# Kernel optimization log

Measured on AMD Instinct MI355X. Metric: run time of the kernel, lower is better.

Reference implementation:

```python
import jax, jax.numpy as jnp
import numpy as np

B, C, H, W = 32, 3, 512, 512


def setup_inputs() -> dict:
    key = jax.random.key(0)
    k_img, k_mask = jax.random.split(key)
    image = jax.random.normal(k_img, (B, C, H, W), dtype=jnp.float32)
    # mask values: 0 -> pepper (set 0.0), 1 -> salt (set 1.0), 2 -> keep pixel
    mask = jax.random.randint(k_mask, (B, 1, H, W), 0, 3, dtype=jnp.int32)
    return {"image": image, "mask": mask}


def reference(image, mask):
    # mask (B,1,H,W) broadcasts over channels, matching repeat(1, C, 1, 1).
    # Single fused elementwise pass: 0 where mask==0, 1 where mask==1, else image.
    out = jnp.where(mask == 0, jnp.float32(0.0),
                    jnp.where(mask == 1, jnp.float32(1.0), image))
    return out
```

## Files before the change

kernel.cpp:

```cpp
#include <hip/hip_runtime.h>


constexpr int B  = 32;
constexpr int C  = 3;
constexpr int HW = 512 * 512;
constexpr int G_PER_PLANE = HW / 4;
constexpr int TOTAL_G = B * C * G_PER_PLANE;
constexpr int U = 4;
constexpr int BLOCK = 256;
constexpr int G_PER_BLOCK = BLOCK * U;

typedef float nt_f4 __attribute__((ext_vector_type(4)));
typedef int   nt_i4 __attribute__((ext_vector_type(4)));

__global__ __launch_bounds__(BLOCK)
void sp_kernel(const float* __restrict__ img,
               const int*   __restrict__ mask,
               float*       __restrict__ out) {
    const int base = blockIdx.x * G_PER_BLOCK + threadIdx.x;

    int   t[U];
    nt_i4 m[U];
    nt_f4 v[U];

    #pragma unroll
    for (int k = 0; k < U; ++k) {
        t[k] = base + k * BLOCK;
        const int plane = t[k] >> 16;
        const int b     = plane / 3;
        const int g     = t[k] & (G_PER_PLANE - 1);
        m[k] = *(const nt_i4*)(mask + (size_t)b * HW + (size_t)g * 4);
        v[k] = *(const nt_f4*)(img + (size_t)t[k] * 4);
    }

    #pragma unroll
    for (int k = 0; k < U; ++k) {
        nt_f4 r;
        r.x = (m[k].x == 0) ? 0.0f : ((m[k].x == 1) ? 1.0f : v[k].x);
        r.y = (m[k].y == 0) ? 0.0f : ((m[k].y == 1) ? 1.0f : v[k].y);
        r.z = (m[k].z == 0) ? 0.0f : ((m[k].z == 1) ? 1.0f : v[k].z);
        r.w = (m[k].w == 0) ? 0.0f : ((m[k].w == 1) ? 1.0f : v[k].w);
        __builtin_nontemporal_store(r, (nt_f4*)(out + (size_t)t[k] * 4));
    }
}

extern "C" void kernel_launch(void* const* d_in, const int* in_sizes, int n_in,
                              void* d_out, int out_size, void* d_ws, size_t ws_size,
                              hipStream_t stream) {
    const float* img  = (const float*)d_in[0];
    const int*   mask = (const int*)d_in[1];
    float*       out  = (float*)d_out;

    const int grid = TOTAL_G / G_PER_BLOCK;
    sp_kernel<<<grid, BLOCK, 0, stream>>>(img, mask, out);
}
```

Baseline: 201.6 us.

## Use fixed 2048-block grid with per-thread loop and plain stores

Replaces the one-tile-per-block launch (6144 blocks) with a fixed grid of 2048 blocks, each looping over three unrolled tiles of four float4 groups per thread. This cuts block scheduling overhead and gives each thread more independent loads in flight. It also swaps the nontemporal output stores for ordinary stores. That may change cache behaviour for the 100MB write stream and could add L2 pollution.

```diff
diff --git a/kernel.cpp b/kernel.cpp
--- a/kernel.cpp
+++ b/kernel.cpp
@@ -6,41 +6,46 @@
 constexpr int HW = 512 * 512;
 constexpr int G_PER_PLANE = HW / 4;
 constexpr int TOTAL_G = B * C * G_PER_PLANE;
-constexpr int U = 4;
-constexpr int BLOCK = 256;
-constexpr int G_PER_BLOCK = BLOCK * U;
+constexpr int BLOCK   = 256;
+constexpr int GRID    = 2048;
+constexpr int G_PER_BLOCK = TOTAL_G / GRID;
+constexpr int U       = 4;
+constexpr int ITERS   = G_PER_BLOCK / (BLOCK * U);
 
-typedef float nt_f4 __attribute__((ext_vector_type(4)));
-typedef int   nt_i4 __attribute__((ext_vector_type(4)));
+typedef float f4 __attribute__((ext_vector_type(4)));
+typedef int   i4 __attribute__((ext_vector_type(4)));
 
 __global__ __launch_bounds__(BLOCK)
 void sp_kernel(const float* __restrict__ img,
                const int*   __restrict__ mask,
                float*       __restrict__ out) {
-    const int base = blockIdx.x * G_PER_BLOCK + threadIdx.x;
-
-    int   t[U];
-    nt_i4 m[U];
-    nt_f4 v[U];
+    const int blockBase = blockIdx.x * G_PER_BLOCK + threadIdx.x;
 
     #pragma unroll
-    for (int k = 0; k < U; ++k) {
-        t[k] = base + k * BLOCK;
-        const int plane = t[k] >> 16;
-        const int b     = plane / 3;
-        const int g     = t[k] & (G_PER_PLANE - 1);
-        m[k] = *(const nt_i4*)(mask + (size_t)b * HW + (size_t)g * 4);
-        v[k] = *(const nt_f4*)(img + (size_t)t[k] * 4);
-    }
+    for (int i = 0; i < ITERS; ++i) {
+        int t[U];
+        i4  m[U];
+        f4  v[U];
 
-    #pragma unroll
-    for (int k = 0; k < U; ++k) {
-        nt_f4 r;
-        r.x = (m[k].x == 0) ? 0.0f : ((m[k].x == 1) ? 1.0f : v[k].x);
-        r.y = (m[k].y == 0) ? 0.0f : ((m[k].y == 1) ? 1.0f : v[k].y);
-        r.z = (m[k].z == 0) ? 0.0f : ((m[k].z == 1) ? 1.0f : v[k].z);
-        r.w = (m[k].w == 0) ? 0.0f : ((m[k].w == 1) ? 1.0f : v[k].w);
-        __builtin_nontemporal_store(r, (nt_f4*)(out + (size_t)t[k] * 4));
+        #pragma unroll
+        for (int k = 0; k < U; ++k) {
+            t[k] = blockBase + (i * U + k) * BLOCK;
+            const int plane = t[k] >> 16;
+            const int b     = plane / 3;
+            const int g     = t[k] & (G_PER_PLANE - 1);
+            m[k] = *(const i4*)(mask + (size_t)b * HW + (size_t)g * 4);
+            v[k] = *(const f4*)(img + (size_t)t[k] * 4);
+        }
+
+        #pragma unroll
+        for (int k = 0; k < U; ++k) {
+            f4 r;
+            r.x = (m[k].x == 0) ? 0.0f : ((m[k].x == 1) ? 1.0f : v[k].x);
+            r.y = (m[k].y == 0) ? 0.0f : ((m[k].y == 1) ? 1.0f : v[k].y);
+            r.z = (m[k].z == 0) ? 0.0f : ((m[k].z == 1) ? 1.0f : v[k].z);
+            r.w = (m[k].w == 0) ? 0.0f : ((m[k].w == 1) ? 1.0f : v[k].w);
+            *(f4*)(out + (size_t)t[k] * 4) = r;
+        }
     }
 }
 
@@ -51,6 +56,5 @@
     const int*   mask = (const int*)d_in[1];
     float*       out  = (float*)d_out;
 
-    const int grid = TOTAL_G / G_PER_BLOCK;
-    sp_kernel<<<grid, BLOCK, 0, stream>>>(img, mask, out);
+    sp_kernel<<<GRID, BLOCK, 0, stream>>>(img, mask, out);
 }
```

Result: no change. 205.1 us (+1.7%).
